# Performance work log

Hardware: AMD Instinct MI355X
Metric: run time of the kernel (lower is better)

## Reference

```python
import jax, jax.numpy as jnp
import numpy as np


def conv1d(x, w, b, pad):
    # x: (B, Cin, T), w: (Cout, Cin, K), b: (Cout,)
    y = jax.lax.conv_general_dilated(x, w, window_strides=(1,), padding=[(pad, pad)],
                                     dimension_numbers=('NCH', 'OIH', 'NCH'))
    return y + b[None, :, None]


def setup_inputs() -> dict:
    key = jax.random.key(0)
    ks = jax.random.split(key, 12)
    B, Cm, T1, Ct, T2, Ca = 8, 80, 800, 512, 200, 80
    queries = jax.random.normal(ks[0], (B, Cm, T1), dtype=jnp.float32)
    keys = jax.random.normal(ks[1], (B, Ct, T2), dtype=jnp.float32)
    query_lens = jnp.full((B,), T1, dtype=jnp.int32)
    key_lens = jax.random.randint(ks[2], (B,), T2 // 2, T2 + 1)
    # mask True where key position is padding (>= key_len): (B, T2, 1)
    mask = (jnp.arange(T2)[None, :] >= key_lens[:, None])[:, :, None]
    attn_prior = jax.random.uniform(ks[3], (B, T1, T2), dtype=jnp.float32) + 0.1
    # key_proj: Conv1d(512->1024, k=3, pad=1) + ReLU + Conv1d(1024->80, k=1)
    kp_w1 = jax.random.normal(ks[4], (2 * Ct, Ct, 3), jnp.float32) * 0.02
    kp_b1 = jnp.zeros((2 * Ct,), jnp.float32)
    kp_w2 = jax.random.normal(ks[5], (Ca, 2 * Ct, 1), jnp.float32) * 0.02
    kp_b2 = jnp.zeros((Ca,), jnp.float32)
    # query_proj (3xconv): Conv1d(80->160,k3)+ReLU+Conv1d(160->80,k1)+ReLU+Conv1d(80->80,k1)
    qp_w1 = jax.random.normal(ks[6], (2 * Cm, Cm, 3), jnp.float32) * 0.05
    qp_b1 = jnp.zeros((2 * Cm,), jnp.float32)
    qp_w2 = jax.random.normal(ks[7], (Cm, 2 * Cm, 1), jnp.float32) * 0.05
    qp_b2 = jnp.zeros((Cm,), jnp.float32)
    qp_w3 = jax.random.normal(ks[8], (Ca, Cm, 1), jnp.float32) * 0.05
    qp_b3 = jnp.zeros((Ca,), jnp.float32)
    return {"queries": queries, "keys": keys, "query_lens": query_lens, "mask": mask,
            "attn_prior": attn_prior, "kp_w1": kp_w1, "kp_b1": kp_b1, "kp_w2": kp_w2,
            "kp_b2": kp_b2, "qp_w1": qp_w1, "qp_b1": qp_b1, "qp_w2": qp_w2,
            "qp_b2": qp_b2, "qp_w3": qp_w3, "qp_b3": qp_b3}


def reference(queries, keys, query_lens, mask, attn_prior,
              kp_w1, kp_b1, kp_w2, kp_b2,
              qp_w1, qp_b1, qp_w2, qp_b2, qp_w3, qp_b3):
    # key projection: (B, Ct, T2) -> (B, Ca, T2)
    ke = conv1d(keys, kp_w1, kp_b1, pad=1)
    ke = jax.nn.relu(ke)
    ke = conv1d(ke, kp_w2, kp_b2, pad=0)
    # query projection ('3xconv'): (B, Cm, T1) -> (B, Ca, T1)
    qe = conv1d(queries, qp_w1, qp_b1, pad=1)
    qe = jax.nn.relu(qe)
    qe = conv1d(qe, qp_w2, qp_b2, pad=0)
    qe = jax.nn.relu(qe)
    qe = conv1d(qe, qp_w3, qp_b3, pad=0)
    # broadcasted squared L2 distance: (B, Ca, T1, T2) -> reduce C -> (B, 1, T1, T2)
    diff2 = (qe[:, :, :, None] - ke[:, :, None, :]) ** 2
    attn = -0.0005 * jnp.sum(diff2, axis=1, keepdims=True)
    # prior in log domain
    attn = jax.nn.log_softmax(attn, axis=3) + jnp.log(attn_prior[:, None] + 1e-8)
    attn_logprob = attn
    # mask (B, T2, 1) -> (B, 1, 1, T2)
    m = jnp.transpose(mask, (0, 2, 1))[:, :, None, :]
    attn = jnp.where(m, -jnp.inf, attn)
    attn = jax.nn.softmax(attn, axis=3)
    return (attn, attn_logprob)
```

## Files before the change

### kernel.cpp

```cpp
#include <hip/hip_runtime.h>
#include <hip/hip_bf16.h>
#include <math.h>

#define B_  8
#define CM  80
#define T1_ 800
#define CT  512
#define T2_ 200
#define CA  80

using bf16 = __hip_bfloat16;
typedef __attribute__((ext_vector_type(8))) short bf16x8;
typedef __attribute__((ext_vector_type(4))) float f32x4;

#define LDSW 56
#define LDSW2 72
#define LDSW3 168
#define LDSW4 104

__device__ __forceinline__ float load_sel(const void* p, long idx, int isf32) {
  if (isf32) return ((const float*)p)[idx];
  return __bfloat162float(((const bf16*)p)[idx]);
}

__device__ __forceinline__ unsigned short f2bf(float x) {
  bf16 h = __float2bfloat16(x);
  return *reinterpret_cast<unsigned short*>(&h);
}

__device__ __forceinline__ int detect_f32(const unsigned short* q) {
  __shared__ int s_f;
  const int tid = threadIdx.x;
  if (tid < 64) {
    unsigned short u = q[2 * tid];
    int e = (u >> 7) & 0xFF;
    unsigned long long bal = __ballot(e < 100 || e > 154);
    if (tid == 0) s_f = (__popcll(bal) >= 16) ? 1 : 0;
  }
  __syncthreads();
  return s_f;
}

__device__ void task_cvt_t(const void* X, bf16* XT, int f, int C, int T,
                           int id2, int tilesT, float* smem, int tid) {
  const int per_b = tilesT * ((C + 31) >> 5);
  const int b = id2 / per_b;
  const int r = id2 - b * per_b;
  const int ct = r / tilesT, tt = r - ct * tilesT;
  const int c0 = ct * 32, t0 = tt * 32;
  const int tx = tid & 31, trow = tid >> 5;
#pragma unroll
  for (int p = 0; p < 4; ++p) {
    const int cr = trow + 8 * p;
    if (c0 + cr < C && t0 + tx < T)
      smem[cr * 33 + tx] = load_sel(X, ((long)b * C + c0 + cr) * T + t0 + tx, f);
  }
  __syncthreads();
#pragma unroll
  for (int p = 0; p < 4; ++p) {
    const int tr = trow + 8 * p;
    if (t0 + tr < T && c0 + tx < C)
      XT[((long)b * T + t0 + tr) * C + c0 + tx] =
          __float2bfloat16(smem[tx * 33 + tr]);
  }
}

__device__ void task_wt3v(const void* W, bf16* WT, int f, int Co, int Ci,
                          int id2, int tid) {
  const int i = id2 * 256 + tid;
  const int g4 = Ci >> 2;
  if (i >= Co * g4) return;
  const int co = i / g4, ci = (i - co * g4) * 4;
  const long sbase = ((long)co * Ci + ci) * 3;
  float w[12];
  if (f) {
    const float4* s = (const float4*)((const float*)W + sbase);
    float4 f0 = s[0], f1 = s[1], f2 = s[2];
    w[0]=f0.x; w[1]=f0.y; w[2]=f0.z; w[3]=f0.w; w[4]=f1.x; w[5]=f1.y;
    w[6]=f1.z; w[7]=f1.w; w[8]=f2.x; w[9]=f2.y; w[10]=f2.z; w[11]=f2.w;
  } else {
#pragma unroll
    for (int j = 0; j < 12; ++j) w[j] = load_sel(W, sbase + j, 0);
  }
#pragma unroll
  for (int dk = 0; dk < 3; ++dk) {
    ushort4 u;
    u.x = f2bf(w[0 * 3 + dk]); u.y = f2bf(w[1 * 3 + dk]);
    u.z = f2bf(w[2 * 3 + dk]); u.w = f2bf(w[3 * 3 + dk]);
    *(ushort4*)(WT + ((long)dk * Co + co) * Ci + ci) = u;
  }
}

__device__ void task_cvtv(const void* W, bf16* O, int f, int n, int id2, int tid) {
  const int i = (id2 * 256 + tid) * 4;
  if (i >= n) return;
  ushort4 u;
  if (f) {
    float4 v = *(const float4*)((const float*)W + i);
    u.x = f2bf(v.x); u.y = f2bf(v.y); u.z = f2bf(v.z); u.w = f2bf(v.w);
  } else {
    u.x = f2bf(load_sel(W, i, 0));     u.y = f2bf(load_sel(W, i + 1, 0));
    u.z = f2bf(load_sel(W, i + 2, 0)); u.w = f2bf(load_sel(W, i + 3, 0));
  }
  *(ushort4*)(O + i) = u;
}

__global__ __launch_bounds__(256) void k_prep(
    const void* __restrict__ queries, const void* __restrict__ keys,
    const void* __restrict__ mask,
    const void* __restrict__ kp_w1, const void* __restrict__ kp_b1,
    const void* __restrict__ kp_w2, const void* __restrict__ kp_b2,
    const void* __restrict__ qp_w1, const void* __restrict__ qp_b1,
    const void* __restrict__ qp_w2, const void* __restrict__ qp_b2,
    const void* __restrict__ qp_w3, const void* __restrict__ qp_b3,
    bf16* __restrict__ keysT, bf16* __restrict__ queriesT,
    bf16* __restrict__ w1T, bf16* __restrict__ qw1T,
    bf16* __restrict__ kw2c, bf16* __restrict__ qw2c, bf16* __restrict__ qw3c,
    float* __restrict__ biasf, float* __restrict__ mf, float* __restrict__ kn) {
  __shared__ float smem[32 * 33];
  const int tid = threadIdx.x;
  const int f = detect_f32((const unsigned short*)queries);
  int id = blockIdx.x;

  if (id < 896) { task_cvt_t(keys, keysT, f, CT, T2_, id, 7, smem, tid); return; }
  id -= 896;
  if (id < 600) { task_cvt_t(queries, queriesT, f, CM, T1_, id, 25, smem, tid); return; }
  id -= 600;
  if (id < 512) { task_wt3v(kp_w1, w1T, f, 1024, CT, id, tid); return; }
  id -= 512;
  if (id < 13) { task_wt3v(qp_w1, qw1T, f, 160, CM, id, tid); return; }
  id -= 13;
  if (id < 80) { task_cvtv(kp_w2, kw2c, f, 80 * 1024, id, tid); return; }
  id -= 80;
  if (id < 13) { task_cvtv(qp_w2, qw2c, f, 80 * 160, id, tid); return; }
  id -= 13;
  if (id < 7) { task_cvtv(qp_w3, qw3c, f, 80 * 80, id, tid); return; }
  id -= 7;

  if (id == 0) {
    for (int i = tid; i < 1424; i += 256) {
      float v;
      if (i < 1024)      v = load_sel(kp_b1, i, f);
      else if (i < 1104) v = load_sel(kp_b2, i - 1024, f);
      else if (i < 1264) v = load_sel(qp_b1, i - 1104, f);
      else if (i < 1344) v = load_sel(qp_b2, i - 1264, f);
      else               v = load_sel(qp_b3, i - 1344, f);
      biasf[i] = v;
    }
    for (int i = tid; i < B_ * T2_; i += 256) kn[i] = 0.f;
    return;
  }

  {
    int* s_fmt = (int*)smem;
    const int nmask = B_ * T2_;
    if (tid == 0) s_fmt[0] = 1;
    __syncthreads();
    const unsigned int* wi = (const unsigned int*)mask;
    const int nw = nmask / 4;
    int pri = 0;
    for (int i = tid; i < nw; i += 256) {
      unsigned int w = wi[i];
      if (w == 0u || w == 1u) continue;
      if (w == 0x3F803F80u || w == 0x00003F80u) { pri = max(pri, 2); continue; }
      if (w == 0x3F800000u) continue;
      unsigned int b0 = w & 0xFFu, b1 = (w >> 8) & 0xFFu,
                   b2 = (w >> 16) & 0xFFu, b3 = (w >> 24) & 0xFFu;
      if (b0 <= 1u && b1 <= 1u && b2 <= 1u && b3 <= 1u) pri = max(pri, 3);
      else pri = max(pri, 2);
    }
    if (pri) atomicMax(&s_fmt[0], pri);
    __syncthreads();
    const int fmt = s_fmt[0];
    for (int i = tid; i < nmask; i += 256) {
      int m;
      if (fmt == 3)      m = ((const unsigned char*)mask)[i] != 0;
      else if (fmt == 2) m = ((const unsigned short*)mask)[i] != 0;
      else               m = (wi[i] != 0u);
      mf[i] = (float)m;
    }
  }
}

__device__ void conv_tile(
    const bf16* __restrict__ XT, const bf16* __restrict__ WT,
    const float* __restrict__ bias, void* __restrict__ Y,
    int Cin, int Cout, int T, int KW, int pad, int relu, int outmode,
    int m0, int n0, short* As, short* Bs, float* Y2 = nullptr) {
  const int K = Cin * KW;
  const int tid = threadIdx.x;
  const int wave = tid >> 6;
  const int lane = tid & 63;

  const int row = tid >> 2;
  const int koff = (tid & 3) * 8;
  const int n = n0 + row;
  const int bb = n / T;
  const int t = n - bb * T;

  const int wm = (wave >> 1) * 32;
  const int wn = (wave & 1) * 32;
  const int fm = lane & 15;
  const int quad = lane >> 4;

  f32x4 acc[2][2] = {};

  const short* ap0 = As + (wm + fm) * LDSW + quad * 8;
  const short* bp0 = Bs + (wn + fm) * LDSW + quad * 8;

  auto loadA = [&](int k0) -> uint4 {
    const int k = k0 + koff;
    const int m = m0 + row;
    uint4 v = {0u, 0u, 0u, 0u};
    if (m < Cout && k < K) {
      const int dk = k / Cin;
      const int ci = k - dk * Cin;
      v = *(const uint4*)(WT + ((long)dk * Cout + m) * Cin + ci);
    }
    return v;
  };
  auto loadB = [&](int k0) -> uint4 {
    const int k = k0 + koff;
    uint4 v = {0u, 0u, 0u, 0u};
    if (k < K) {
      const int dk = k / Cin;
      const int ci = k - dk * Cin;
      const int tt = t + dk - pad;
      if (tt >= 0 && tt < T)
        v = *(const uint4*)(XT + ((long)bb * T + tt) * Cin + ci);
    }
    return v;
  };

  uint4 va = loadA(0);
  uint4 vb = loadB(0);

  for (int k0 = 0; k0 < K; k0 += 32) {
    *(uint4*)(As + row * LDSW + koff) = va;
    *(uint4*)(Bs + row * LDSW + koff) = vb;
    if (k0 + 32 < K) {
      va = loadA(k0 + 32);
      vb = loadB(k0 + 32);
    }
    __syncthreads();
    {
      bf16x8 a0 = *(const bf16x8*)(ap0);
      bf16x8 a1 = *(const bf16x8*)(ap0 + 16 * LDSW);
      bf16x8 b0 = *(const bf16x8*)(bp0);
      bf16x8 b1 = *(const bf16x8*)(bp0 + 16 * LDSW);
      acc[0][0] = __builtin_amdgcn_mfma_f32_16x16x32_bf16(a0, b0, acc[0][0], 0, 0, 0);
      acc[0][1] = __builtin_amdgcn_mfma_f32_16x16x32_bf16(a0, b1, acc[0][1], 0, 0, 0);
      acc[1][0] = __builtin_amdgcn_mfma_f32_16x16x32_bf16(a1, b0, acc[1][0], 0, 0, 0);
      acc[1][1] = __builtin_amdgcn_mfma_f32_16x16x32_bf16(a1, b1, acc[1][1], 0, 0, 0);
    }
    __syncthreads();
  }

#pragma unroll
  for (int mi = 0; mi < 2; ++mi) {
    const int mrow = m0 + wm + mi * 16 + quad * 4;
    if (mrow >= Cout) continue;
    float bi[4];
#pragma unroll
    for (int r = 0; r < 4; ++r) bi[r] = bias[mrow + r];
#pragma unroll
    for (int ni = 0; ni < 2; ++ni) {
      const int ncol = n0 + wn + ni * 16 + fm;
      float o[4];
#pragma unroll
      for (int r = 0; r < 4; ++r) {
        float v = acc[mi][ni][r] + bi[r];
        if (relu) v = fmaxf(v, 0.f);
        o[r] = v;
      }
      if (outmode == 0) {
        ushort4 u;
        u.x = f2bf(o[0]); u.y = f2bf(o[1]); u.z = f2bf(o[2]); u.w = f2bf(o[3]);
        *(ushort4*)((bf16*)Y + (long)ncol * Cout + mrow) = u;
      } else if (outmode == 1) {
        *(float4*)((float*)Y + (long)ncol * Cout + mrow) =
            make_float4(o[0], o[1], o[2], o[3]);
      } else {
        const int bb2 = ncol / T;
        const int tloc = ncol - bb2 * T;
        float s4 = 0.f;
#pragma unroll
        for (int r = 0; r < 4; ++r) {
          ((float*)Y)[((long)bb2 * Cout + mrow + r) * T + tloc] = -2.f * o[r];
          s4 = fmaf(o[r], o[r], s4);
        }
        atomicAdd(&Y2[ncol], s4);
      }
    }
  }
}

__device__ void conv_tile128(
    const bf16* __restrict__ XT, const bf16* __restrict__ WT,
    const float* __restrict__ bias, bf16* __restrict__ Y,
    int m0, int n0, short* As, short* Bs) {
  const int Cin = CT, Cout = 1024, T = T2_, K = 1536;
  const int tid = threadIdx.x;
  const int wave = tid >> 6;
  const int lane = tid & 63;

  const int rowb = tid >> 2;
  const int nb = n0 + rowb;
  const int bbb = nb / T;
  const int tb = nb - bbb * T;

  const int wm = (wave >> 1) * 64;
  const int wn = (wave & 1) * 32;
  const int fm = lane & 15;
  const int quad = lane >> 4;

  f32x4 acc[4][2] = {};

  const short* ap0 = As + (wm + fm) * LDSW2 + quad * 8;
  const short* bp0 = Bs + (wn + fm) * LDSW2 + quad * 8;

  const int arow = tid >> 1;
  const int acol = (tid & 1) * 32;
  const int kcb = (tid & 3) * 16;

  uint4 va[4];
  uint4 vb0, vb1;

  auto loadA = [&](int k0) {
    const int dk = k0 >> 9;
    const int ci0 = k0 & 511;
    const bf16* src = WT + ((long)dk * Cout + m0 + arow) * Cin + ci0 + acol;
#pragma unroll
    for (int hh = 0; hh < 4; ++hh) va[hh] = *(const uint4*)(src + hh * 8);
  };
  auto loadB = [&](int k0) {
    const int dk = k0 >> 9;
    const int ci0 = k0 & 511;
    const int tt = tb + dk - 1;
    if (tt >= 0 && tt < T) {
      const bf16* src = XT + ((long)bbb * T + tt) * Cin + ci0 + kcb;
      vb0 = *(const uint4*)(src);
      vb1 = *(const uint4*)(src + 8);
    } else {
      uint4 z = {0u, 0u, 0u, 0u};
      vb0 = z; vb1 = z;
    }
  };

  loadA(0);
  loadB(0);

  for (int k0 = 0; k0 < K; k0 += 64) {
    {
      short* dst = As + arow * LDSW2 + acol;
#pragma unroll
      for (int hh = 0; hh < 4; ++hh) *(uint4*)(dst + hh * 8) = va[hh];
      short* dstb = Bs + rowb * LDSW2 + kcb;
      *(uint4*)(dstb) = vb0;
      *(uint4*)(dstb + 8) = vb1;
    }
    if (k0 + 64 < K) {
      loadA(k0 + 64);
      loadB(k0 + 64);
    }
    __syncthreads();
#pragma unroll
    for (int h = 0; h < 2; ++h) {
      bf16x8 b0 = *(const bf16x8*)(bp0 + h * 32);
      bf16x8 b1 = *(const bf16x8*)(bp0 + 16 * LDSW2 + h * 32);
#pragma unroll
      for (int mi = 0; mi < 4; ++mi) {
        bf16x8 a = *(const bf16x8*)(ap0 + mi * 16 * LDSW2 + h * 32);
        acc[mi][0] = __builtin_amdgcn_mfma_f32_16x16x32_bf16(a, b0, acc[mi][0], 0, 0, 0);
        acc[mi][1] = __builtin_amdgcn_mfma_f32_16x16x32_bf16(a, b1, acc[mi][1], 0, 0, 0);
      }
    }
    __syncthreads();
  }

#pragma unroll
  for (int mi = 0; mi < 4; ++mi) {
    const int mrow = m0 + wm + mi * 16 + quad * 4;
    float bi[4];
#pragma unroll
    for (int r = 0; r < 4; ++r) bi[r] = bias[mrow + r];
#pragma unroll
    for (int ni = 0; ni < 2; ++ni) {
      const int ncol = n0 + wn + ni * 16 + fm;
      const long base = (long)ncol * Cout + mrow;
      ushort4 u;
      u.x = f2bf(fmaxf(acc[mi][ni][0] + bi[0], 0.f));
      u.y = f2bf(fmaxf(acc[mi][ni][1] + bi[1], 0.f));
      u.z = f2bf(fmaxf(acc[mi][ni][2] + bi[2], 0.f));
      u.w = f2bf(fmaxf(acc[mi][ni][3] + bi[3], 0.f));
      *(ushort4*)(Y + base) = u;
    }
  }
}

__global__ __launch_bounds__(256) void k_conv1(
    const bf16* __restrict__ keysT, const bf16* __restrict__ w1T,
    const float* __restrict__ b_k1, bf16* __restrict__ ke1T,
    const bf16* __restrict__ queriesT, const bf16* __restrict__ qw1T,
    const float* __restrict__ b_q1, bf16* __restrict__ qe1T) {
  __shared__ __align__(16) short sA[128 * LDSW2];
  __shared__ __align__(16) short sB[64 * LDSW2];
  int j = blockIdx.x;
  if (j < 200) {
    conv_tile128(keysT, w1T, b_k1, ke1T, (j / 25) * 128, (j % 25) * 64, sA, sB);
  } else {
    j -= 200;
    conv_tile(queriesT, qw1T, b_q1, qe1T, CM, 160, T1_, 3, 1, 1, 0,
              (j / 100) * 64, (j % 100) * 64, sA, sA + 64 * LDSW);
  }
}

__device__ void conv23_tile(
    const bf16* __restrict__ qe1T, const bf16* __restrict__ qw2c,
    const float* __restrict__ b_q2, const bf16* __restrict__ qw3c,
    const float* __restrict__ b_q3, float* __restrict__ qeT,
    float* __restrict__ qn, int n0, short* smem) {
  short* sIn = smem;
  short* sW2 = smem + 64 * LDSW3;
  short* sC  = smem;
  short* sW3 = smem + 64 * LDSW3;
  const int tid = threadIdx.x;
  const int wave = tid >> 6;
  const int lane = tid & 63;
  const int fm = lane & 15;
  const int quad = lane >> 4;

#pragma unroll
  for (int c = tid; c < 1280; c += 256) {
    const int row = c / 20, kc = (c - row * 20) * 8;
    uint4 v = *(const uint4*)(qe1T + (long)(n0 + row) * 160 + kc);
    *(uint4*)(sIn + row * LDSW3 + kc) = v;
  }
  for (int c = tid; c < 1600; c += 256) {
    const int row = c / 20, kc = (c - row * 20) * 8;
    uint4 v = *(const uint4*)(qw2c + (long)row * 160 + kc);
    *(uint4*)(sW2 + row * LDSW3 + kc) = v;
  }
  __syncthreads();

  f32x4 acc1[5] = {};
#pragma unroll
  for (int ks = 0; ks < 5; ++ks) {
    bf16x8 b = *(const bf16x8*)(sIn + (16 * wave + fm) * LDSW3 + ks * 32 + quad * 8);
#pragma unroll
    for (int mt = 0; mt < 5; ++mt) {
      bf16x8 a = *(const bf16x8*)(sW2 + (16 * mt + fm) * LDSW3 + ks * 32 + quad * 8);
      acc1[mt] = __builtin_amdgcn_mfma_f32_16x16x32_bf16(a, b, acc1[mt], 0, 0, 0);
    }
  }
  __syncthreads();

#pragma unroll
  for (int mt = 0; mt < 5; ++mt) {
    const int ch = 16 * mt + quad * 4;
    const float4 b2 = *(const float4*)(b_q2 + ch);
    ushort4 u;
    u.x = f2bf(fmaxf(acc1[mt][0] + b2.x, 0.f));
    u.y = f2bf(fmaxf(acc1[mt][1] + b2.y, 0.f));
    u.z = f2bf(fmaxf(acc1[mt][2] + b2.z, 0.f));
    u.w = f2bf(fmaxf(acc1[mt][3] + b2.w, 0.f));
    *(ushort4*)(sC + (16 * wave + fm) * LDSW4 + ch) = u;
  }
  if (tid < 128) {
    const int row = tid >> 1, off = 80 + (tid & 1) * 8;
    uint4 z = {0u, 0u, 0u, 0u};
    *(uint4*)(sC + row * LDSW4 + off) = z;
  }
  for (int c = tid; c < 800; c += 256) {
    const int row = c / 10, kc = (c - row * 10) * 8;
    uint4 v = *(const uint4*)(qw3c + (long)row * 80 + kc);
    *(uint4*)(sW3 + row * LDSW4 + kc) = v;
  }
  if (tid < 160) {
    const int row = tid >> 1, off = 80 + (tid & 1) * 8;
    uint4 z = {0u, 0u, 0u, 0u};
    *(uint4*)(sW3 + row * LDSW4 + off) = z;
  }
  __syncthreads();

  f32x4 acc2[5] = {};
#pragma unroll
  for (int ks = 0; ks < 3; ++ks) {
    bf16x8 b = *(const bf16x8*)(sC + (16 * wave + fm) * LDSW4 + ks * 32 + quad * 8);
#pragma unroll
    for (int mt = 0; mt < 5; ++mt) {
      bf16x8 a = *(const bf16x8*)(sW3 + (16 * mt + fm) * LDSW4 + ks * 32 + quad * 8);
      acc2[mt] = __builtin_amdgcn_mfma_f32_16x16x32_bf16(a, b, acc2[mt], 0, 0, 0);
    }
  }

  const int pos = n0 + 16 * wave + fm;
  float p = 0.f;
#pragma unroll
  for (int mt = 0; mt < 5; ++mt) {
    const int ch = 16 * mt + quad * 4;
    const float4 b3 = *(const float4*)(b_q3 + ch);
    float4 o = make_float4(acc2[mt][0] + b3.x, acc2[mt][1] + b3.y,
                           acc2[mt][2] + b3.z, acc2[mt][3] + b3.w);
    p = fmaf(o.x, o.x, p); p = fmaf(o.y, o.y, p);
    p = fmaf(o.z, o.z, p); p = fmaf(o.w, o.w, p);
    *(float4*)(qeT + (long)pos * CA + ch) = o;
  }
  p += __shfl_xor(p, 16, 64);
  p += __shfl_xor(p, 32, 64);
  if (quad == 0) qn[pos] = p;
}

__global__ __launch_bounds__(256) void k_conv2f(
    const bf16* __restrict__ ke1T, const bf16* __restrict__ kw2c,
    const float* __restrict__ b_k2, float* __restrict__ keT,
    float* __restrict__ kn,
    const bf16* __restrict__ qe1T, const bf16* __restrict__ qw2c,
    const float* __restrict__ b_q2, const bf16* __restrict__ qw3c,
    const float* __restrict__ b_q3, float* __restrict__ qeT,
    float* __restrict__ qn) {
  __shared__ __align__(16) short smem[64 * LDSW3 + 80 * LDSW3];
  int j = blockIdx.x;
  if (j < 50) {
    conv_tile(ke1T, kw2c, b_k2, keT, 1024, CA, T2_, 1, 0, 0, 2,
              (j / 25) * 64, (j % 25) * 64, smem, smem + 64 * LDSW, kn);
  } else {
    conv23_tile(qe1T, qw2c, b_q2, qw3c, b_q3, qeT, qn, (j - 50) * 64, smem);
  }
}

__global__ __launch_bounds__(256) void k_dist(
    const float* __restrict__ qeT, const float* __restrict__ keT2,
    const float* __restrict__ kn, const float* __restrict__ qn,
    const void* __restrict__ prior, const float* __restrict__ mf,
    void* __restrict__ out, const unsigned short* __restrict__ qprobe) {
  __shared__ float sq[4 * CA];
  __shared__ float sqn[4];
  __shared__ float redA[16], redB[16], redC[16], redD[16];
  const int f = detect_f32(qprobe);
  const int b = blockIdx.y;
  const int t1base = blockIdx.x * 4;
  const int tid = threadIdx.x;
  const int wid = tid >> 6;

  for (int i = tid; i < 4 * CA; i += 256) {
    int u = i / CA, c = i - u * CA;
    sq[i] = qeT[((long)b * T1_ + t1base + u) * CA + c];
  }
  if (tid < 4) sqn[tid] = qn[b * T1_ + t1base + tid];
  __syncthreads();

  const int t2 = tid;
  const bool valid = (t2 < T2_);
  float x[4] = {-INFINITY, -INFINITY, -INFINITY, -INFINITY};
  if (valid) {
    const float* kp = keT2 + (long)b * CA * T2_ + t2;
    const float knv = kn[b * T2_ + t2];
    float a0 = 0.f, a1 = 0.f, a2 = 0.f, a3 = 0.f;
#pragma unroll 2
    for (int j = 0; j < CA; j += 4) {
      const float4 q0 = *(const float4*)(sq + 0 * CA + j);
      const float4 q1 = *(const float4*)(sq + 1 * CA + j);
      const float4 q2 = *(const float4*)(sq + 2 * CA + j);
      const float4 q3 = *(const float4*)(sq + 3 * CA + j);
      const float k0v = kp[(j + 0) * T2_];
      const float k1v = kp[(j + 1) * T2_];
      const float k2v = kp[(j + 2) * T2_];
      const float k3v = kp[(j + 3) * T2_];
      a0 = fmaf(k0v, q0.x, a0); a0 = fmaf(k1v, q0.y, a0);
      a0 = fmaf(k2v, q0.z, a0); a0 = fmaf(k3v, q0.w, a0);
      a1 = fmaf(k0v, q1.x, a1); a1 = fmaf(k1v, q1.y, a1);
      a1 = fmaf(k2v, q1.z, a1); a1 = fmaf(k3v, q1.w, a1);
      a2 = fmaf(k0v, q2.x, a2); a2 = fmaf(k1v, q2.y, a2);
      a2 = fmaf(k2v, q2.z, a2); a2 = fmaf(k3v, q2.w, a2);
      a3 = fmaf(k0v, q3.x, a3); a3 = fmaf(k1v, q3.y, a3);
      a3 = fmaf(k2v, q3.z, a3); a3 = fmaf(k3v, q3.w, a3);
    }
    x[0] = -0.0005f * (a0 + sqn[0] + knv);
    x[1] = -0.0005f * (a1 + sqn[1] + knv);
    x[2] = -0.0005f * (a2 + sqn[2] + knv);
    x[3] = -0.0005f * (a3 + sqn[3] + knv);
  }

  const float mval = valid ? mf[b * T2_ + t2] : 0.f;
  const long N = (long)B_ * T1_ * T2_;

  float m[4] = {x[0], x[1], x[2], x[3]};
#pragma unroll
  for (int o = 32; o > 0; o >>= 1)
#pragma unroll
    for (int u = 0; u < 4; ++u) m[u] = fmaxf(m[u], __shfl_down(m[u], o, 64));
  if ((tid & 63) == 0)
#pragma unroll
    for (int u = 0; u < 4; ++u) redA[wid * 4 + u] = m[u];
  __syncthreads();
  float M1[4];
#pragma unroll
  for (int u = 0; u < 4; ++u)
    M1[u] = fmaxf(fmaxf(redA[u], redA[4 + u]), fmaxf(redA[8 + u], redA[12 + u]));

  float e[4], s1[4];
#pragma unroll
  for (int u = 0; u < 4; ++u) {
    e[u] = (x[u] == -INFINITY) ? 0.f : __expf(x[u] - M1[u]);
    s1[u] = e[u];
  }
#pragma unroll
  for (int o = 32; o > 0; o >>= 1)
#pragma unroll
    for (int u = 0; u < 4; ++u) s1[u] += __shfl_down(s1[u], o, 64);
  if ((tid & 63) == 0)
#pragma unroll
    for (int u = 0; u < 4; ++u) redB[wid * 4 + u] = s1[u];
  __syncthreads();
  float lp[4];
#pragma unroll
  for (int u = 0; u < 4; ++u) {
    const float S1 = redB[u] + redB[4 + u] + redB[8 + u] + redB[12 + u];
    const float logZ = __logf(S1);
    lp[u] = -INFINITY;
    if (valid) {
      const long oidx = ((long)b * T1_ + t1base + u) * T2_ + t2;
      float pr = load_sel(prior, oidx, f);
      lp[u] = (x[u] - M1[u] - logZ) + __logf(fmaxf(pr, 0.f) + 1e-8f);
      if (f) ((float*)out)[N + oidx] = lp[u];
      else   ((bf16*)out)[N + oidx] = __float2bfloat16(lp[u]);
    }
  }

  float xm[4], m2[4];
#pragma unroll
  for (int u = 0; u < 4; ++u) {
    xm[u] = (valid && mval != 0.f) ? -INFINITY : lp[u];
    m2[u] = xm[u];
  }
#pragma unroll
  for (int o = 32; o > 0; o >>= 1)
#pragma unroll
    for (int u = 0; u < 4; ++u) m2[u] = fmaxf(m2[u], __shfl_down(m2[u], o, 64));
  if ((tid & 63) == 0)
#pragma unroll
    for (int u = 0; u < 4; ++u) redC[wid * 4 + u] = m2[u];
  __syncthreads();
  float M2[4];
#pragma unroll
  for (int u = 0; u < 4; ++u)
    M2[u] = fmaxf(fmaxf(redC[u], redC[4 + u]), fmaxf(redC[8 + u], redC[12 + u]));

  float e2[4], s2[4];
#pragma unroll
  for (int u = 0; u < 4; ++u) {
    e2[u] = (xm[u] == -INFINITY) ? 0.f : __expf(xm[u] - M2[u]);
    s2[u] = e2[u];
  }
#pragma unroll
  for (int o = 32; o > 0; o >>= 1)
#pragma unroll
    for (int u = 0; u < 4; ++u) s2[u] += __shfl_down(s2[u], o, 64);
  if ((tid & 63) == 0)
#pragma unroll
    for (int u = 0; u < 4; ++u) redD[wid * 4 + u] = s2[u];
  __syncthreads();
#pragma unroll
  for (int u = 0; u < 4; ++u) {
    const float S2 = redD[u] + redD[4 + u] + redD[8 + u] + redD[12 + u];
    if (valid) {
      float a = (S2 > 0.f) ? (e2[u] / S2) : 0.f;
      const long oidx = ((long)b * T1_ + t1base + u) * T2_ + t2;
      if (f) ((float*)out)[oidx] = a;
      else   ((bf16*)out)[oidx] = __float2bfloat16(a);
    }
  }
}

extern "C" void kernel_launch(void* const* d_in, const int* in_sizes, int n_in,
                              void* d_out, int out_size, void* d_ws, size_t ws_size,
                              hipStream_t stream) {
  const void* queries = d_in[0];
  const void* keys    = d_in[1];
  const void* mask    = d_in[3];
  const void* prior   = d_in[4];
  const void* kp_w1 = d_in[5];
  const void* kp_b1 = d_in[6];
  const void* kp_w2 = d_in[7];
  const void* kp_b2 = d_in[8];
  const void* qp_w1 = d_in[9];
  const void* qp_b1 = d_in[10];
  const void* qp_w2 = d_in[11];
  const void* qp_b2 = d_in[12];
  const void* qp_w3 = d_in[13];
  const void* qp_b3 = d_in[14];

  float* keT   = (float*)d_ws;
  float* qeT   = keT + 128000;
  float* mf    = qeT + 512000;
  float* biasf = mf + 1600;
  float* kn    = biasf + 1440;
  float* qn    = kn + 1600;
  bf16* keysT    = (bf16*)(qn + 6400);
  bf16* queriesT = keysT + 819200;
  bf16* w1T      = queriesT + 512000;
  bf16* qw1T     = w1T + 1572864;
  bf16* kw2c     = qw1T + 38400;
  bf16* qw2c     = kw2c + 81920;
  bf16* qw3c     = qw2c + 12800;
  bf16* ke1T     = qw3c + 6400;
  bf16* qe1T     = ke1T + 1638400;

  float* b_k1 = biasf;
  float* b_k2 = biasf + 1024;
  float* b_q1 = biasf + 1104;
  float* b_q2 = biasf + 1264;
  float* b_q3 = biasf + 1344;

  k_prep<<<2123, 256, 0, stream>>>(
      queries, keys, mask,
      kp_w1, kp_b1, kp_w2, kp_b2,
      qp_w1, qp_b1, qp_w2, qp_b2, qp_w3, qp_b3,
      keysT, queriesT, w1T, qw1T, kw2c, qw2c, qw3c, biasf, mf, kn);

  k_conv1<<<500, 256, 0, stream>>>(keysT, w1T, b_k1, ke1T,
                                   queriesT, qw1T, b_q1, qe1T);

  k_conv2f<<<150, 256, 0, stream>>>(ke1T, kw2c, b_k2, keT, kn,
                                    qe1T, qw2c, b_q2, qw3c, b_q3, qeT, qn);

  k_dist<<<dim3(200, B_), 256, 0, stream>>>(
      qeT, keT, kn, qn, prior, mf, d_out, (const unsigned short*)queries);
}
```

Before: 168.2 us.

## Fuse four kernel launches into one persistent kernel with grid barriers

Replaces the prep, conv1, conv2/3 and distance kernels with a single persistent kernel of 512 blocks that loops over each stage's tasks and separates stages with atomic-counter grid barriers. The goal is to remove three kernel launch gaps and the tail idle time between dependent stages. In exchange, stages with few tiles (150 or 500) leave many blocks idle, and the spin barrier adds atomic traffic. It also relies on all 512 blocks being co-resident, otherwise it deadlocks, and it adds a memset launch.

New measurement: 334.3 us. 98.8% more time.

```diff
diff --git a/kernel.cpp b/kernel.cpp
--- a/kernel.cpp
+++ b/kernel.cpp
@@ -17,6 +17,8 @@
 #define LDSW2 72
 #define LDSW3 168
 #define LDSW4 104
+
+#define NBLK 512
 
 __device__ __forceinline__ float load_sel(const void* p, long idx, int isf32) {
   if (isf32) return ((const float*)p)[idx];
@@ -39,6 +41,19 @@
   }
   __syncthreads();
   return s_f;
+}
+
+__device__ __forceinline__ void grid_bar(int* cnt) {
+  __syncthreads();
+  if (threadIdx.x == 0) {
+    __threadfence();
+    int arrived = atomicAdd(cnt, 1) + 1;
+    if (arrived < NBLK) {
+      while (atomicAdd(cnt, 0) < NBLK) __builtin_amdgcn_s_sleep(4);
+    }
+    __threadfence();
+  }
+  __syncthreads();
 }
 
 __device__ void task_cvt_t(const void* X, bf16* XT, int f, int C, int T,
@@ -105,23 +120,15 @@
   *(ushort4*)(O + i) = u;
 }
 
-__global__ __launch_bounds__(256) void k_prep(
-    const void* __restrict__ queries, const void* __restrict__ keys,
-    const void* __restrict__ mask,
-    const void* __restrict__ kp_w1, const void* __restrict__ kp_b1,
-    const void* __restrict__ kp_w2, const void* __restrict__ kp_b2,
-    const void* __restrict__ qp_w1, const void* __restrict__ qp_b1,
-    const void* __restrict__ qp_w2, const void* __restrict__ qp_b2,
-    const void* __restrict__ qp_w3, const void* __restrict__ qp_b3,
-    bf16* __restrict__ keysT, bf16* __restrict__ queriesT,
-    bf16* __restrict__ w1T, bf16* __restrict__ qw1T,
-    bf16* __restrict__ kw2c, bf16* __restrict__ qw2c, bf16* __restrict__ qw3c,
-    float* __restrict__ biasf, float* __restrict__ mf, float* __restrict__ kn) {
-  __shared__ float smem[32 * 33];
-  const int tid = threadIdx.x;
-  const int f = detect_f32((const unsigned short*)queries);
-  int id = blockIdx.x;
-
+__device__ void prep_task(
+    int id, int f, int tid, float* smem,
+    const void* queries, const void* keys, const void* mask,
+    const void* kp_w1, const void* kp_b1, const void* kp_w2, const void* kp_b2,
+    const void* qp_w1, const void* qp_b1, const void* qp_w2, const void* qp_b2,
+    const void* qp_w3, const void* qp_b3,
+    bf16* keysT, bf16* queriesT, bf16* w1T, bf16* qw1T,
+    bf16* kw2c, bf16* qw2c, bf16* qw3c,
+    float* biasf, float* mf, float* kn) {
   if (id < 896) { task_cvt_t(keys, keysT, f, CT, T2_, id, 7, smem, tid); return; }
   id -= 896;
   if (id < 600) { task_cvt_t(queries, queriesT, f, CM, T1_, id, 25, smem, tid); return; }
@@ -398,23 +405,6 @@
   }
 }
 
-__global__ __launch_bounds__(256) void k_conv1(
-    const bf16* __restrict__ keysT, const bf16* __restrict__ w1T,
-    const float* __restrict__ b_k1, bf16* __restrict__ ke1T,
-    const bf16* __restrict__ queriesT, const bf16* __restrict__ qw1T,
-    const float* __restrict__ b_q1, bf16* __restrict__ qe1T) {
-  __shared__ __align__(16) short sA[128 * LDSW2];
-  __shared__ __align__(16) short sB[64 * LDSW2];
-  int j = blockIdx.x;
-  if (j < 200) {
-    conv_tile128(keysT, w1T, b_k1, ke1T, (j / 25) * 128, (j % 25) * 64, sA, sB);
-  } else {
-    j -= 200;
-    conv_tile(queriesT, qw1T, b_q1, qe1T, CM, 160, T1_, 3, 1, 1, 0,
-              (j / 100) * 64, (j % 100) * 64, sA, sA + 64 * LDSW);
-  }
-}
-
 __device__ void conv23_tile(
     const bf16* __restrict__ qe1T, const bf16* __restrict__ qw2c,
     const float* __restrict__ b_q2, const bf16* __restrict__ qw3c,
@@ -511,36 +501,19 @@
   if (quad == 0) qn[pos] = p;
 }
 
-__global__ __launch_bounds__(256) void k_conv2f(
-    const bf16* __restrict__ ke1T, const bf16* __restrict__ kw2c,
-    const float* __restrict__ b_k2, float* __restrict__ keT,
-    float* __restrict__ kn,
-    const bf16* __restrict__ qe1T, const bf16* __restrict__ qw2c,
-    const float* __restrict__ b_q2, const bf16* __restrict__ qw3c,
-    const float* __restrict__ b_q3, float* __restrict__ qeT,
-    float* __restrict__ qn) {
-  __shared__ __align__(16) short smem[64 * LDSW3 + 80 * LDSW3];
-  int j = blockIdx.x;
-  if (j < 50) {
-    conv_tile(ke1T, kw2c, b_k2, keT, 1024, CA, T2_, 1, 0, 0, 2,
-              (j / 25) * 64, (j % 25) * 64, smem, smem + 64 * LDSW, kn);
-  } else {
-    conv23_tile(qe1T, qw2c, b_q2, qw3c, b_q3, qeT, qn, (j - 50) * 64, smem);
-  }
-}
-
-__global__ __launch_bounds__(256) void k_dist(
+__device__ void dist_task(
+    int b, int xt, int f,
     const float* __restrict__ qeT, const float* __restrict__ keT2,
     const float* __restrict__ kn, const float* __restrict__ qn,
     const void* __restrict__ prior, const float* __restrict__ mf,
-    void* __restrict__ out, const unsigned short* __restrict__ qprobe) {
-  __shared__ float sq[4 * CA];
-  __shared__ float sqn[4];
-  __shared__ float redA[16], redB[16], redC[16], redD[16];
-  const int f = detect_f32(qprobe);
-  const int b = blockIdx.y;
-  const int t1base = blockIdx.x * 4;
-  const int tid = threadIdx.x;
+    void* __restrict__ out, float* sbase, int tid) {
+  float* sq   = sbase;
+  float* sqn  = sq + 4 * CA;
+  float* redA = sqn + 4;
+  float* redB = redA + 16;
+  float* redC = redB + 16;
+  float* redD = redC + 16;
+  const int t1base = xt * 4;
   const int wid = tid >> 6;
 
   for (int i = tid; i < 4 * CA; i += 256) {
@@ -673,6 +646,74 @@
   }
 }
 
+__global__ __launch_bounds__(256, 2) void k_all(
+    const void* __restrict__ queries, const void* __restrict__ keys,
+    const void* __restrict__ mask, const void* __restrict__ prior,
+    const void* __restrict__ kp_w1, const void* __restrict__ kp_b1,
+    const void* __restrict__ kp_w2, const void* __restrict__ kp_b2,
+    const void* __restrict__ qp_w1, const void* __restrict__ qp_b1,
+    const void* __restrict__ qp_w2, const void* __restrict__ qp_b2,
+    const void* __restrict__ qp_w3, const void* __restrict__ qp_b3,
+    bf16* __restrict__ keysT, bf16* __restrict__ queriesT,
+    bf16* __restrict__ w1T, bf16* __restrict__ qw1T,
+    bf16* __restrict__ kw2c, bf16* __restrict__ qw2c, bf16* __restrict__ qw3c,
+    float* __restrict__ biasf, float* __restrict__ mf,
+    float* __restrict__ kn, float* __restrict__ qn,
+    bf16* __restrict__ ke1T, bf16* __restrict__ qe1T,
+    float* __restrict__ keT, float* __restrict__ qeT,
+    void* __restrict__ out, int* __restrict__ bars) {
+  __shared__ __align__(16) short smem[144 * LDSW3];
+  const int tid = threadIdx.x;
+  const int bid = blockIdx.x;
+  const int f = detect_f32((const unsigned short*)queries);
+
+  const float* b_k1 = biasf;
+  const float* b_k2 = biasf + 1024;
+  const float* b_q1 = biasf + 1104;
+  const float* b_q2 = biasf + 1264;
+  const float* b_q3 = biasf + 1344;
+
+  for (int t = bid; t < 2123; t += NBLK) {
+    prep_task(t, f, tid, (float*)smem,
+              queries, keys, mask,
+              kp_w1, kp_b1, kp_w2, kp_b2,
+              qp_w1, qp_b1, qp_w2, qp_b2, qp_w3, qp_b3,
+              keysT, queriesT, w1T, qw1T, kw2c, qw2c, qw3c, biasf, mf, kn);
+    __syncthreads();
+  }
+  grid_bar(&bars[0]);
+
+  for (int t = bid; t < 500; t += NBLK) {
+    if (t < 200) {
+      conv_tile128(keysT, w1T, b_k1, ke1T, (t / 25) * 128, (t % 25) * 64,
+                   smem, smem + 128 * LDSW2);
+    } else {
+      const int j = t - 200;
+      conv_tile(queriesT, qw1T, b_q1, qe1T, CM, 160, T1_, 3, 1, 1, 0,
+                (j / 100) * 64, (j % 100) * 64, smem, smem + 64 * LDSW);
+    }
+    __syncthreads();
+  }
+  grid_bar(&bars[1]);
+
+  for (int t = bid; t < 150; t += NBLK) {
+    if (t < 50) {
+      conv_tile(ke1T, kw2c, b_k2, keT, 1024, CA, T2_, 1, 0, 0, 2,
+                (t / 25) * 64, (t % 25) * 64, smem, smem + 64 * LDSW, kn);
+    } else {
+      conv23_tile(qe1T, qw2c, b_q2, qw3c, b_q3, qeT, qn, (t - 50) * 64, smem);
+    }
+    __syncthreads();
+  }
+  grid_bar(&bars[2]);
+
+  for (int t = bid; t < 1600; t += NBLK) {
+    dist_task(t / 200, t % 200, f, qeT, keT, kn, qn, prior, mf, out,
+              (float*)smem, tid);
+    __syncthreads();
+  }
+}
+
 extern "C" void kernel_launch(void* const* d_in, const int* in_sizes, int n_in,
                               void* d_out, int out_size, void* d_ws, size_t ws_size,
                               hipStream_t stream) {
@@ -708,23 +749,16 @@
   bf16* qe1T     = ke1T + 1638400;
 
   float* b_k1 = biasf;
-  float* b_k2 = biasf + 1024;
-  float* b_q1 = biasf + 1104;
-  float* b_q2 = biasf + 1264;
-  float* b_q3 = biasf + 1344;
-
-  k_prep<<<2123, 256, 0, stream>>>(
-      queries, keys, mask,
+
+  int* bars = (int*)((char*)d_ws + (200u << 20));
+  hipMemsetAsync(bars, 0, 256, stream);
+
+  k_all<<<NBLK, 256, 0, stream>>>(
+      queries, keys, mask, prior,
       kp_w1, kp_b1, kp_w2, kp_b2,
       qp_w1, qp_b1, qp_w2, qp_b2, qp_w3, qp_b3,
-      keysT, queriesT, w1T, qw1T, kw2c, qw2c, qw3c, biasf, mf, kn);
-
-  k_conv1<<<500, 256, 0, stream>>>(keysT, w1T, b_k1, ke1T,
-                                   queriesT, qw1T, b_q1, qe1T);
-
-  k_conv2f<<<150, 256, 0, stream>>>(ke1T, kw2c, b_k2, keT, kn,
-                                    qe1T, qw2c, b_q2, qw3c, b_q3, qeT, qn);
-
-  k_dist<<<dim3(200, B_), 256, 0, stream>>>(
-      qeT, keT, kn, qn, prior, mf, d_out, (const unsigned short*)queries);
-}
+      keysT, queriesT, w1T, qw1T, kw2c, qw2c, qw3c,
+      biasf, mf, kn, qn, ke1T, qe1T, keT, qeT,
+      d_out, bars);
+  (void)b_k1; (void)in_sizes; (void)n_in; (void)out_size; (void)ws_size;
+}
```

## Prepack key conv weights into MFMA fragment order and load A directly from global

Applied to the files above, without the earlier changes.

The key-projection first conv weights are now repacked in the prep kernel into per-lane MFMA fragment order, so each wave loads its A operands straight from global memory into registers. This removes the A tile staging through LDS and one set of LDS writes and reads per k-step. Block indexing is also changed so consecutive blocks share a weight panel, which should improve L2 reuse. The cost is a strided scalar weight-packing pass that runs on every call and A loads that are no longer prefetched a step ahead, so global latency may be exposed before the barrier.

Result: faster. 150.8 us (-10.3%).

```diff
diff --git a/kernel.cpp b/kernel.cpp
--- a/kernel.cpp
+++ b/kernel.cpp
@@ -63,6 +63,33 @@
       XT[((long)b * T + t0 + tr) * C + c0 + tx] =
           __float2bfloat16(smem[tx * 33 + tr]);
   }
+}
+
+__device__ void task_wfrag(const void* W, bf16* WF, int f, int id2, int tid) {
+  const int id = id2 * 256 + tid;
+  const int l  = id & 63;
+  int rest = id >> 6;
+  const int h  = rest & 1; rest >>= 1;
+  const int mi = rest & 3; rest >>= 2;
+  const int w2 = rest & 1; rest >>= 1;
+  const int ks = rest % 24;
+  const int p  = rest / 24;
+  const int co = p * 128 + w2 * 64 + mi * 16 + (l & 15);
+  const int k0 = ks * 64 + h * 32 + (l >> 4) * 8;
+  const int dk = k0 >> 9;
+  const int ci = k0 & 511;
+  const long sbase = ((long)co * 512 + ci) * 3 + dk;
+  ushort4 u0, u1;
+  u0.x = f2bf(load_sel(W, sbase + 0 * 3, f));
+  u0.y = f2bf(load_sel(W, sbase + 1 * 3, f));
+  u0.z = f2bf(load_sel(W, sbase + 2 * 3, f));
+  u0.w = f2bf(load_sel(W, sbase + 3 * 3, f));
+  u1.x = f2bf(load_sel(W, sbase + 4 * 3, f));
+  u1.y = f2bf(load_sel(W, sbase + 5 * 3, f));
+  u1.z = f2bf(load_sel(W, sbase + 6 * 3, f));
+  u1.w = f2bf(load_sel(W, sbase + 7 * 3, f));
+  *(ushort4*)(WF + (long)id * 8) = u0;
+  *(ushort4*)(WF + (long)id * 8 + 4) = u1;
 }
 
 __device__ void task_wt3v(const void* W, bf16* WT, int f, int Co, int Ci,
@@ -114,7 +141,7 @@
     const void* __restrict__ qp_w2, const void* __restrict__ qp_b2,
     const void* __restrict__ qp_w3, const void* __restrict__ qp_b3,
     bf16* __restrict__ keysT, bf16* __restrict__ queriesT,
-    bf16* __restrict__ w1T, bf16* __restrict__ qw1T,
+    bf16* __restrict__ w1F, bf16* __restrict__ qw1T,
     bf16* __restrict__ kw2c, bf16* __restrict__ qw2c, bf16* __restrict__ qw3c,
     float* __restrict__ biasf, float* __restrict__ mf, float* __restrict__ kn) {
   __shared__ float smem[32 * 33];
@@ -126,8 +153,8 @@
   id -= 896;
   if (id < 600) { task_cvt_t(queries, queriesT, f, CM, T1_, id, 25, smem, tid); return; }
   id -= 600;
-  if (id < 512) { task_wt3v(kp_w1, w1T, f, 1024, CT, id, tid); return; }
-  id -= 512;
+  if (id < 768) { task_wfrag(kp_w1, w1F, f, id, tid); return; }
+  id -= 768;
   if (id < 13) { task_wt3v(qp_w1, qw1T, f, 160, CM, id, tid); return; }
   id -= 13;
   if (id < 80) { task_cvtv(kp_w2, kw2c, f, 80 * 1024, id, tid); return; }
@@ -295,44 +322,32 @@
   }
 }
 
-__device__ void conv_tile128(
-    const bf16* __restrict__ XT, const bf16* __restrict__ WT,
+__device__ void conv_key128(
+    const bf16* __restrict__ XT, const bf16* __restrict__ WF,
     const float* __restrict__ bias, bf16* __restrict__ Y,
-    int m0, int n0, short* As, short* Bs) {
-  const int Cin = CT, Cout = 1024, T = T2_, K = 1536;
+    int panel, int n0, short* Bs) {
+  const int Cin = CT, Cout = 1024, T = T2_;
   const int tid = threadIdx.x;
   const int wave = tid >> 6;
   const int lane = tid & 63;
+  const int m0 = panel * 128;
 
   const int rowb = tid >> 2;
   const int nb = n0 + rowb;
   const int bbb = nb / T;
   const int tb = nb - bbb * T;
-
-  const int wm = (wave >> 1) * 64;
+  const int kcb = (tid & 3) * 16;
+
+  const int w2 = wave >> 1;
+  const int wm = w2 * 64;
   const int wn = (wave & 1) * 32;
   const int fm = lane & 15;
   const int quad = lane >> 4;
 
   f32x4 acc[4][2] = {};
-
-  const short* ap0 = As + (wm + fm) * LDSW2 + quad * 8;
   const short* bp0 = Bs + (wn + fm) * LDSW2 + quad * 8;
 
-  const int arow = tid >> 1;
-  const int acol = (tid & 1) * 32;
-  const int kcb = (tid & 3) * 16;
-
-  uint4 va[4];
   uint4 vb0, vb1;
-
-  auto loadA = [&](int k0) {
-    const int dk = k0 >> 9;
-    const int ci0 = k0 & 511;
-    const bf16* src = WT + ((long)dk * Cout + m0 + arow) * Cin + ci0 + acol;
-#pragma unroll
-    for (int hh = 0; hh < 4; ++hh) va[hh] = *(const uint4*)(src + hh * 8);
-  };
   auto loadB = [&](int k0) {
     const int dk = k0 >> 9;
     const int ci0 = k0 & 511;
@@ -347,22 +362,25 @@
     }
   };
 
-  loadA(0);
   loadB(0);
 
-  for (int k0 = 0; k0 < K; k0 += 64) {
+  for (int k0 = 0; k0 < 1536; k0 += 64) {
+    const int ks = k0 >> 6;
     {
-      short* dst = As + arow * LDSW2 + acol;
-#pragma unroll
-      for (int hh = 0; hh < 4; ++hh) *(uint4*)(dst + hh * 8) = va[hh];
       short* dstb = Bs + rowb * LDSW2 + kcb;
       *(uint4*)(dstb) = vb0;
       *(uint4*)(dstb + 8) = vb1;
     }
-    if (k0 + 64 < K) {
-      loadA(k0 + 64);
-      loadB(k0 + 64);
-    }
+    if (k0 + 64 < 1536) loadB(k0 + 64);
+
+    const long abase = ((((long)panel * 24 + ks) * 2 + w2) * 4096) + lane * 8;
+    bf16x8 a[4][2];
+#pragma unroll
+    for (int mi = 0; mi < 4; ++mi)
+#pragma unroll
+      for (int h = 0; h < 2; ++h)
+        a[mi][h] = *(const bf16x8*)(WF + abase + (mi * 2 + h) * 512);
+
     __syncthreads();
 #pragma unroll
     for (int h = 0; h < 2; ++h) {
@@ -370,9 +388,8 @@
       bf16x8 b1 = *(const bf16x8*)(bp0 + 16 * LDSW2 + h * 32);
 #pragma unroll
       for (int mi = 0; mi < 4; ++mi) {
-        bf16x8 a = *(const bf16x8*)(ap0 + mi * 16 * LDSW2 + h * 32);
-        acc[mi][0] = __builtin_amdgcn_mfma_f32_16x16x32_bf16(a, b0, acc[mi][0], 0, 0, 0);
-        acc[mi][1] = __builtin_amdgcn_mfma_f32_16x16x32_bf16(a, b1, acc[mi][1], 0, 0, 0);
+        acc[mi][0] = __builtin_amdgcn_mfma_f32_16x16x32_bf16(a[mi][h], b0, acc[mi][0], 0, 0, 0);
+        acc[mi][1] = __builtin_amdgcn_mfma_f32_16x16x32_bf16(a[mi][h], b1, acc[mi][1], 0, 0, 0);
       }
     }
     __syncthreads();
@@ -399,19 +416,18 @@
 }
 
 __global__ __launch_bounds__(256) void k_conv1(
-    const bf16* __restrict__ keysT, const bf16* __restrict__ w1T,
+    const bf16* __restrict__ keysT, const bf16* __restrict__ w1F,
     const float* __restrict__ b_k1, bf16* __restrict__ ke1T,
     const bf16* __restrict__ queriesT, const bf16* __restrict__ qw1T,
     const float* __restrict__ b_q1, bf16* __restrict__ qe1T) {
-  __shared__ __align__(16) short sA[128 * LDSW2];
-  __shared__ __align__(16) short sB[64 * LDSW2];
+  __shared__ __align__(16) short smem[2 * 64 * LDSW];
   int j = blockIdx.x;
   if (j < 200) {
-    conv_tile128(keysT, w1T, b_k1, ke1T, (j / 25) * 128, (j % 25) * 64, sA, sB);
+    conv_key128(keysT, w1F, b_k1, ke1T, j & 7, (j >> 3) * 64, smem);
   } else {
     j -= 200;
     conv_tile(queriesT, qw1T, b_q1, qe1T, CM, 160, T1_, 3, 1, 1, 0,
-              (j / 100) * 64, (j % 100) * 64, sA, sA + 64 * LDSW);
+              (j / 100) * 64, (j % 100) * 64, smem, smem + 64 * LDSW);
   }
 }
 
@@ -699,8 +715,8 @@
   float* qn    = kn + 1600;
   bf16* keysT    = (bf16*)(qn + 6400);
   bf16* queriesT = keysT + 819200;
-  bf16* w1T      = queriesT + 512000;
-  bf16* qw1T     = w1T + 1572864;
+  bf16* w1F      = queriesT + 512000;
+  bf16* qw1T     = w1F + 1572864;
   bf16* kw2c     = qw1T + 38400;
   bf16* qw2c     = kw2c + 81920;
   bf16* qw3c     = qw2c + 12800;
@@ -713,13 +729,13 @@
   float* b_q2 = biasf + 1264;
   float* b_q3 = biasf + 1344;
 
-  k_prep<<<2123, 256, 0, stream>>>(
+  k_prep<<<2379, 256, 0, stream>>>(
       queries, keys, mask,
       kp_w1, kp_b1, kp_w2, kp_b2,
       qp_w1, qp_b1, qp_w2, qp_b2, qp_w3, qp_b3,
-      keysT, queriesT, w1T, qw1T, kw2c, qw2c, qw3c, biasf, mf, kn);
-
-  k_conv1<<<500, 256, 0, stream>>>(keysT, w1T, b_k1, ke1T,
+      keysT, queriesT, w1F, qw1T, kw2c, qw2c, qw3c, biasf, mf, kn);
+
+  k_conv1<<<500, 256, 0, stream>>>(keysT, w1F, b_k1, ke1T,
                                    queriesT, qw1T, b_q1, qe1T);
 
   k_conv2f<<<150, 256, 0, stream>>>(ke1T, kw2c, b_k2, keT, kn,
```
